# Kernel tuning notes

Hardware: AMD Instinct MI355X
Metric: run time of the kernel (lower is better)

The kernel has to match this reference:

```python
import jax, jax.numpy as jnp
import numpy as np

B, T, D_MODEL, D_HEAD = 4, 2048, 1024, 64

def setup_inputs() -> dict:
    key = jax.random.key(0)
    k1, k2, k3, k4 = jax.random.split(key, 4)
    x = jax.random.normal(k1, (B, T, D_MODEL), dtype=jnp.float32)
    # Linear(d_model, d_head) weights stored as [d_model, d_head] for x @ W
    s = 1.0 / np.sqrt(D_MODEL)
    W_Q = jax.random.normal(k2, (D_MODEL, D_HEAD), dtype=jnp.float32) * s
    W_K = jax.random.normal(k3, (D_MODEL, D_HEAD), dtype=jnp.float32) * s
    W_V = jax.random.normal(k4, (D_MODEL, D_HEAD), dtype=jnp.float32) * s
    return {"x": x, "W_Q": W_Q, "W_K": W_K, "W_V": W_V}

def reference(x, W_Q, W_K, W_V):
    d_head = W_Q.shape[-1]
    Q = jnp.einsum('btm,md->btd', x, W_Q)
    K = jnp.einsum('btm,md->btd', x, W_K)
    V = jnp.einsum('btm,md->btd', x, W_V)
    A = jnp.einsum('bid,bjd->bij', Q, K) / jnp.sqrt(jnp.asarray(d_head, x.dtype))
    T_ = x.shape[1]
    causal = jnp.tril(jnp.ones((T_, T_), dtype=bool))  # [T, T]
    A = jnp.where(causal, A, -jnp.inf)
    A = jax.nn.softmax(A, axis=-1)
    return jnp.einsum('bij,bjd->bid', A, V)
```

## Files before the change

### kernel.cpp

```cpp
#include <hip/hip_runtime.h>
#include <hip/hip_bf16.h>

#define NB 4
#define NT 2048
#define DM 1024
#define DH 64

typedef __attribute__((ext_vector_type(8))) short bf16x8;
typedef __attribute__((ext_vector_type(4))) float f32x4;
typedef unsigned short u16;
typedef unsigned int u32;

static __device__ __forceinline__ u16 f2b(float f) {
    __hip_bfloat16 h = __float2bfloat16(f);
    return __builtin_bit_cast(u16, h);
}
static __device__ __forceinline__ float b2f(u16 h) {
    return __builtin_bit_cast(float, (u32)h << 16);
}
static __device__ __forceinline__ void gld16(const void* g, void* l) {
    __builtin_amdgcn_global_load_lds((const __attribute__((address_space(1))) void*)g,
                                     (__attribute__((address_space(3))) void*)l, 16, 0, 0);
}

__global__ __launch_bounds__(256) void wt_conv(
    const float* __restrict__ WQ, const float* __restrict__ WK,
    const float* __restrict__ WV, u16* __restrict__ wt)
{
    __shared__ u16 tl[64][68];
    const int which = blockIdx.y, kt = blockIdx.x;
    const float* W = (which == 0) ? WQ : (which == 1) ? WK : WV;
    #pragma unroll
    for (int i = 0; i < 4; ++i) {
        int r = (threadIdx.x >> 4) + i * 16;
        int c = (threadIdx.x & 15) * 4;
        float4 v = *(const float4*)&W[(size_t)(kt * 64 + r) * DH + c];
        tl[r][c] = f2b(v.x); tl[r][c + 1] = f2b(v.y);
        tl[r][c + 2] = f2b(v.z); tl[r][c + 3] = f2b(v.w);
    }
    __syncthreads();
    int d = threadIdx.x >> 2, kc = (threadIdx.x & 3) * 16;
    u16 buf[16];
    #pragma unroll
    for (int j = 0; j < 16; ++j) buf[j] = tl[kc + j][d];
    u16* dst = wt + which * 65536 + d * 1024 + kt * 64 + kc;
    *(uint4*)dst = *(uint4*)&buf[0];
    *(uint4*)(dst + 8) = *(uint4*)&buf[8];
}

__global__ __launch_bounds__(256) void qkv_gemm(
    const float* __restrict__ x, const u16* __restrict__ wt,
    u16* __restrict__ Qb, u16* __restrict__ Kb, u16* __restrict__ Vt)
{
    __shared__ float xs[2][4096];
    __shared__ u16 wsm[2][4096];
    const int tid = threadIdx.x, lane = tid & 63, w = tid >> 6;
    const int l15 = lane & 15, g = lane >> 4;
    const int row0 = blockIdx.x * 64;
    const int which = blockIdx.y;
    const u16* Wg = wt + which * 65536;

    auto stage = [&](int kt, int bi) {
        #pragma unroll
        for (int i = 0; i < 4; ++i) {
            u32 D = (u32)(w * 4096 + i * 1024 + lane * 16);
            u32 r = D >> 8, c = D & 255;
            u32 cs = c ^ ((r & 7) << 5);
            gld16(x + (size_t)(row0 + r) * DM + kt * 64 + (cs >> 2),
                  (char*)&xs[bi][0] + w * 4096 + i * 1024);
        }
        #pragma unroll
        for (int i = 0; i < 2; ++i) {
            u32 D = (u32)(w * 2048 + i * 1024 + lane * 16);
            u32 r = D >> 7, c = D & 127;
            u32 cs = c ^ ((r & 7) << 4);
            gld16(Wg + (size_t)r * 1024 + kt * 64 + (cs >> 1),
                  (char*)&wsm[bi][0] + w * 2048 + i * 1024);
        }
    };

    f32x4 acc[4];
    #pragma unroll
    for (int i = 0; i < 4; ++i) acc[i] = {0.f, 0.f, 0.f, 0.f};

    stage(0, 0);
    __syncthreads();

    const int arow = w * 16 + l15;
    for (int kt = 0; kt < 16; ++kt) {
        const int cur = kt & 1;
        if (kt < 15) stage(kt + 1, cur ^ 1);
        const char* xb = (const char*)&xs[cur][0];
        const char* wb = (const char*)&wsm[cur][0];
        #pragma unroll
        for (int ks = 0; ks < 2; ++ks) {
            u32 abase = (u32)(arow * 256 + ks * 128 + g * 32);
            f32x4 a0 = *(const f32x4*)(xb + (abase ^ ((arow & 7) << 5)));
            f32x4 a1 = *(const f32x4*)(xb + ((abase + 16) ^ ((arow & 7) << 5)));
            bf16x8 afrag;
            #pragma unroll
            for (int e = 0; e < 4; ++e) afrag[e] = (short)f2b(a0[e]);
            #pragma unroll
            for (int e = 0; e < 4; ++e) afrag[4 + e] = (short)f2b(a1[e]);
            #pragma unroll
            for (int nt = 0; nt < 4; ++nt) {
                int brow = nt * 16 + l15;
                u32 bb = (u32)(brow * 128 + ks * 64 + g * 16);
                bf16x8 bfrag = *(const bf16x8*)(wb + (bb ^ ((brow & 7) << 4)));
                acc[nt] = __builtin_amdgcn_mfma_f32_16x16x32_bf16(afrag, bfrag, acc[nt], 0, 0, 0);
            }
        }
        __syncthreads();
    }
    #pragma unroll
    for (int nt = 0; nt < 4; ++nt) {
        int dcol = nt * 16 + l15;
        #pragma unroll
        for (int r = 0; r < 4; ++r) {
            int row = row0 + w * 16 + g * 4 + r;
            float v = acc[nt][r];
            if (which == 0)      Qb[(size_t)row * DH + dcol] = f2b(v * 0.125f);
            else if (which == 1) Kb[(size_t)row * DH + dcol] = f2b(v);
            else { int bb2 = row >> 11, t = row & 2047;
                   Vt[(size_t)bb2 * DH * NT + (size_t)dcol * NT + t] = f2b(v); }
        }
    }
}

__global__ __launch_bounds__(256) void attn(
    const u16* __restrict__ Qb, const u16* __restrict__ Kb,
    const u16* __restrict__ Vt, u16* __restrict__ pO, float* __restrict__ pml,
    int CHUNK, int SLOTS)
{
    __shared__ u16 k_lds[2][4096];
    __shared__ u16 v_lds[2][4096];
    __shared__ u16 p_lds[4][16 * 72];

    const int tid = threadIdx.x, lane = tid & 63, w = tid >> 6;
    const int l15 = lane & 15, g = lane >> 4;
    const int b = blockIdx.y;

    int flat = blockIdx.x, qb = 0, nc;
    for (;;) { nc = (qb + CHUNK) / CHUNK; if (flat < nc) break; flat -= nc; ++qb; }
    const int chunk = flat;
    const int t0 = chunk * CHUNK;
    const int t1 = min(t0 + CHUNK, qb + 1);
    const int q0 = qb * 64;

    const u16* Qg = Qb + ((size_t)b * NT + q0 + w * 16) * DH;
    const u16* Kg = Kb + (size_t)b * NT * DH;
    const u16* Vg = Vt + (size_t)b * DH * NT;

    auto stage = [&](int t, int bi) {
        const int j0 = t * 64;
        #pragma unroll
        for (int i = 0; i < 2; ++i) {
            u32 D = (u32)(w * 2048 + i * 1024 + lane * 16);
            u32 r = D >> 7, c = D & 127;
            u32 cs = c ^ ((r & 7) << 4);
            gld16(Kg + (size_t)(j0 + r) * DH + (cs >> 1),
                  (char*)&k_lds[bi][0] + w * 2048 + i * 1024);
            gld16(Vg + (size_t)r * NT + j0 + (cs >> 1),
                  (char*)&v_lds[bi][0] + w * 2048 + i * 1024);
        }
    };

    stage(t0, 0);

    bf16x8 qf[2];
    qf[0] = *(const bf16x8*)(Qg + l15 * DH + g * 8);
    qf[1] = *(const bf16x8*)(Qg + l15 * DH + 32 + g * 8);

    float m_run[4], l_run[4];
    f32x4 oacc[4];
    #pragma unroll
    for (int r = 0; r < 4; ++r) { m_run[r] = -INFINITY; l_run[r] = 0.f; }
    #pragma unroll
    for (int nt = 0; nt < 4; ++nt) oacc[nt] = {0.f, 0.f, 0.f, 0.f};

    __syncthreads();

    for (int t = t0; t < t1; ++t) {
        const int cur = (t - t0) & 1;
        if (t + 1 < t1) stage(t + 1, cur ^ 1);
        const char* kb = (const char*)&k_lds[cur][0];
        const char* vb = (const char*)&v_lds[cur][0];

        f32x4 sacc[4];
        #pragma unroll
        for (int nt = 0; nt < 4; ++nt) sacc[nt] = {0.f, 0.f, 0.f, 0.f};
        __builtin_amdgcn_s_setprio(1);
        #pragma unroll
        for (int ks = 0; ks < 2; ++ks) {
            #pragma unroll
            for (int nt = 0; nt < 4; ++nt) {
                int brow = nt * 16 + l15;
                u32 bb = (u32)(brow * 128 + ks * 64 + g * 16);
                bf16x8 bf = *(const bf16x8*)(kb + (bb ^ ((brow & 7) << 4)));
                sacc[nt] = __builtin_amdgcn_mfma_f32_16x16x32_bf16(qf[ks], bf, sacc[nt], 0, 0, 0);
            }
        }
        __builtin_amdgcn_s_setprio(0);
        if (t == qb) {
            #pragma unroll
            for (int nt = 0; nt < 4; ++nt) {
                int j_local = nt * 16 + l15;
                #pragma unroll
                for (int r = 0; r < 4; ++r) {
                    int q_local = w * 16 + g * 4 + r;
                    if (j_local > q_local) sacc[nt][r] = -1e30f;
                }
            }
        }
        float p[4][4];
        #pragma unroll
        for (int r = 0; r < 4; ++r) {
            float mx = fmaxf(fmaxf(sacc[0][r], sacc[1][r]), fmaxf(sacc[2][r], sacc[3][r]));
            mx = fmaxf(mx, __shfl_xor(mx, 1));
            mx = fmaxf(mx, __shfl_xor(mx, 2));
            mx = fmaxf(mx, __shfl_xor(mx, 4));
            mx = fmaxf(mx, __shfl_xor(mx, 8));
            float m_new = fmaxf(m_run[r], mx);
            float alpha = __expf(m_run[r] - m_new);
            float ps = 0.f;
            #pragma unroll
            for (int nt = 0; nt < 4; ++nt) {
                float pv = __expf(sacc[nt][r] - m_new);
                p[nt][r] = pv; ps += pv;
            }
            ps += __shfl_xor(ps, 1); ps += __shfl_xor(ps, 2);
            ps += __shfl_xor(ps, 4); ps += __shfl_xor(ps, 8);
            l_run[r] = l_run[r] * alpha + ps;
            m_run[r] = m_new;
            #pragma unroll
            for (int nt = 0; nt < 4; ++nt) oacc[nt][r] *= alpha;
        }
        u16* pw = p_lds[w];
        #pragma unroll
        for (int r = 0; r < 4; ++r) {
            int qrow = g * 4 + r;
            #pragma unroll
            for (int nt = 0; nt < 4; ++nt)
                pw[qrow * 72 + nt * 16 + l15] = f2b(p[nt][r]);
        }
        __builtin_amdgcn_s_setprio(1);
        #pragma unroll
        for (int ks = 0; ks < 2; ++ks) {
            bf16x8 pa = *(const bf16x8*)((const char*)pw + (l15 * 144 + ks * 64 + g * 16));
            #pragma unroll
            for (int nt = 0; nt < 4; ++nt) {
                int drow = nt * 16 + l15;
                u32 bb = (u32)(drow * 128 + ks * 64 + g * 16);
                bf16x8 vf = *(const bf16x8*)(vb + (bb ^ ((drow & 7) << 4)));
                oacc[nt] = __builtin_amdgcn_mfma_f32_16x16x32_bf16(pa, vf, oacc[nt], 0, 0, 0);
            }
        }
        __builtin_amdgcn_s_setprio(0);
        __syncthreads();
    }

    const int slot = (b * 32 + qb) * SLOTS + chunk;
    u16* Op = pO + (size_t)slot * 4096;
    #pragma unroll
    for (int nt = 0; nt < 4; ++nt)
        #pragma unroll
        for (int r = 0; r < 4; ++r)
            Op[(w * 16 + g * 4 + r) * 64 + nt * 16 + l15] = f2b(oacc[nt][r]);
    if (l15 == 0) {
        float* mlp = pml + (size_t)slot * 128;
        #pragma unroll
        for (int r = 0; r < 4; ++r) {
            int row = w * 16 + g * 4 + r;
            mlp[row * 2]     = m_run[r];
            mlp[row * 2 + 1] = l_run[r];
        }
    }
}

__global__ __launch_bounds__(256) void merge(
    const u16* __restrict__ pO, const float* __restrict__ pml,
    float* __restrict__ out, int CHUNK, int SLOTS)
{
    int idx = blockIdx.x * 256 + threadIdx.x;
    int row = idx >> 6, d = idx & 63;
    int b = row >> 11, q = row & 2047;
    int qb = q >> 6, rl = q & 63;
    int nc = (qb + CHUNK) / CHUNK;
    int base = (b * 32 + qb) * SLOTS;
    float m = -INFINITY;
    for (int c = 0; c < nc; ++c)
        m = fmaxf(m, pml[(size_t)(base + c) * 128 + rl * 2]);
    float osum = 0.f, lsum = 0.f;
    for (int c = 0; c < nc; ++c) {
        float mc = pml[(size_t)(base + c) * 128 + rl * 2];
        float lc = pml[(size_t)(base + c) * 128 + rl * 2 + 1];
        float wgt = __expf(mc - m);
        osum += wgt * b2f(pO[(size_t)(base + c) * 4096 + rl * 64 + d]);
        lsum += wgt * lc;
    }
    out[idx] = osum / lsum;
}

extern "C" void kernel_launch(void* const* d_in, const int* in_sizes, int n_in,
                              void* d_out, int out_size, void* d_ws, size_t ws_size,
                              hipStream_t stream) {
    const float* x  = (const float*)d_in[0];
    const float* WQ = (const float*)d_in[1];
    const float* WK = (const float*)d_in[2];
    const float* WV = (const float*)d_in[3];
    float* out = (float*)d_out;

    char* ws = (char*)d_ws;
    u16* Qb = (u16*)ws;
    u16* Kb = (u16*)(ws + 1048576);
    u16* Vt = (u16*)(ws + 2097152);
    u16* Wt = (u16*)(ws + 3145728);
    int CHUNK, SLOTS;
    if (ws_size >= 9830400) { CHUNK = 6;  SLOTS = 6; }
    else                    { CHUNK = 16; SLOTS = 2; }
    u16*   pO  = (u16*)(ws + 3145728);
    float* pml = (float*)(ws + 3145728 + (size_t)NB * 32 * SLOTS * 4096 * 2);

    int gx = 0;
    for (int qb = 0; qb < 32; ++qb) gx += (qb + CHUNK) / CHUNK;

    wt_conv<<<dim3(16, 3), 256, 0, stream>>>(WQ, WK, WV, Wt);
    qkv_gemm<<<dim3(128, 3), 256, 0, stream>>>(x, Wt, Qb, Kb, Vt);
    attn<<<dim3(gx, NB), 256, 0, stream>>>(Qb, Kb, Vt, pO, pml, CHUNK, SLOTS);
    merge<<<2048, 256, 0, stream>>>(pO, pml, out, CHUNK, SLOTS);
}
```

Baseline: 48.09 us.

## Deepen QKV GEMM to triple-buffered prefetch with explicit vmcnt waits and barriers

The QKV projection moves from double to triple buffering, prefetching two k-tiles ahead. Each iteration waits on a partial vmcnt so only the tile about to be consumed must have landed, and uses raw s_barrier plus a sched_barrier instead of __syncthreads, which drains all outstanding loads. The attention kernel gets the same partial-wait pattern so the next K/V tile's loads stay in flight, and the GEMM MFMA section runs at raised wave priority. In exchange it uses more LDS per block, which may lower occupancy, and correctness depends on the hand-counted vmcnt values matching the number of issued loads.

```diff
diff --git a/kernel.cpp b/kernel.cpp
--- a/kernel.cpp
+++ b/kernel.cpp
@@ -22,6 +22,8 @@
     __builtin_amdgcn_global_load_lds((const __attribute__((address_space(1))) void*)g,
                                      (__attribute__((address_space(3))) void*)l, 16, 0, 0);
 }
+#define BAR() __builtin_amdgcn_s_barrier()
+#define SBAR() __builtin_amdgcn_sched_barrier(0)
 
 __global__ __launch_bounds__(256) void wt_conv(
     const float* __restrict__ WQ, const float* __restrict__ WK,
@@ -52,8 +54,8 @@
     const float* __restrict__ x, const u16* __restrict__ wt,
     u16* __restrict__ Qb, u16* __restrict__ Kb, u16* __restrict__ Vt)
 {
-    __shared__ float xs[2][4096];
-    __shared__ u16 wsm[2][4096];
+    __shared__ float xs[3][4096];
+    __shared__ u16 wsm[3][4096];
     const int tid = threadIdx.x, lane = tid & 63, w = tid >> 6;
     const int l15 = lane & 15, g = lane >> 4;
     const int row0 = blockIdx.x * 64;
@@ -84,14 +86,19 @@
     for (int i = 0; i < 4; ++i) acc[i] = {0.f, 0.f, 0.f, 0.f};
 
     stage(0, 0);
-    __syncthreads();
+    stage(1, 1);
 
     const int arow = w * 16 + l15;
+    #pragma unroll
     for (int kt = 0; kt < 16; ++kt) {
-        const int cur = kt & 1;
-        if (kt < 15) stage(kt + 1, cur ^ 1);
-        const char* xb = (const char*)&xs[cur][0];
-        const char* wb = (const char*)&wsm[cur][0];
+        if (kt + 2 < 16) stage(kt + 2, (kt + 2) % 3);
+        if (kt < 14)       asm volatile("s_waitcnt vmcnt(12)" ::: "memory");
+        else if (kt == 14) asm volatile("s_waitcnt vmcnt(6)" ::: "memory");
+        else               asm volatile("s_waitcnt vmcnt(0)" ::: "memory");
+        BAR();
+        SBAR();
+        const char* xb = (const char*)&xs[kt % 3][0];
+        const char* wb = (const char*)&wsm[kt % 3][0];
         #pragma unroll
         for (int ks = 0; ks < 2; ++ks) {
             u32 abase = (u32)(arow * 256 + ks * 128 + g * 32);
@@ -102,6 +109,7 @@
             for (int e = 0; e < 4; ++e) afrag[e] = (short)f2b(a0[e]);
             #pragma unroll
             for (int e = 0; e < 4; ++e) afrag[4 + e] = (short)f2b(a1[e]);
+            __builtin_amdgcn_s_setprio(1);
             #pragma unroll
             for (int nt = 0; nt < 4; ++nt) {
                 int brow = nt * 16 + l15;
@@ -109,8 +117,9 @@
                 bf16x8 bfrag = *(const bf16x8*)(wb + (bb ^ ((brow & 7) << 4)));
                 acc[nt] = __builtin_amdgcn_mfma_f32_16x16x32_bf16(afrag, bfrag, acc[nt], 0, 0, 0);
             }
-        }
-        __syncthreads();
+            __builtin_amdgcn_s_setprio(0);
+        }
+        BAR();
     }
     #pragma unroll
     for (int nt = 0; nt < 4; ++nt) {
@@ -178,11 +187,16 @@
     #pragma unroll
     for (int nt = 0; nt < 4; ++nt) oacc[nt] = {0.f, 0.f, 0.f, 0.f};
 
-    __syncthreads();
-
     for (int t = t0; t < t1; ++t) {
         const int cur = (t - t0) & 1;
-        if (t + 1 < t1) stage(t + 1, cur ^ 1);
+        if (t + 1 < t1) {
+            stage(t + 1, cur ^ 1);
+            asm volatile("s_waitcnt vmcnt(4)" ::: "memory");
+        } else {
+            asm volatile("s_waitcnt vmcnt(0)" ::: "memory");
+        }
+        BAR();
+        SBAR();
         const char* kb = (const char*)&k_lds[cur][0];
         const char* vb = (const char*)&v_lds[cur][0];
 
@@ -256,7 +270,7 @@
             }
         }
         __builtin_amdgcn_s_setprio(0);
-        __syncthreads();
+        BAR();
     }
 
     const int slot = (b * 32 + qb) * SLOTS + chunk;
```

Result: no change. 48.26 us (+0.4%).
